# Kernel tuning notes

Measured on AMD Instinct MI355X. Metric: run time of the kernel, lower is better.

## Reference

```python
import jax, jax.numpy as jnp
import numpy as np

B, C, H, W = 8, 512, 32, 32
HEADS, GROUPS, EPS = 8, 32, 1e-5


def setup_inputs() -> dict:
    key = jax.random.key(0)
    ks = jax.random.split(key, 8)
    s = 1.0 / np.sqrt(C)
    return {
        "hidden_states": jax.random.normal(ks[0], (B, C, H, W), jnp.float32),
        "gn_w": jnp.ones((C,), jnp.float32),
        "gn_b": jnp.zeros((C,), jnp.float32),
        "Wq": jax.random.normal(ks[1], (C, C), jnp.float32) * s,
        "Wk": jax.random.normal(ks[2], (C, C), jnp.float32) * s,
        "Wv": jax.random.normal(ks[3], (C, C), jnp.float32) * s,
        "Wo": jax.random.normal(ks[4], (C, C), jnp.float32) * s,
        "bo": jnp.zeros((C,), jnp.float32),
    }


def reference(hidden_states, gn_w, gn_b, Wq, Wk, Wv, Wo, bo):
    b, c, h, w = hidden_states.shape
    S = h * w
    d = c // HEADS
    # [B,C,H,W] -> [B,S,C]
    x = hidden_states.reshape(b, c, S).transpose(0, 2, 1)

    # GroupNorm over channels (applied on [B,C,S] layout): normalize per (group, spatial)
    xt = x.transpose(0, 2, 1).reshape(b, GROUPS, c // GROUPS, S)
    mu = jnp.mean(xt, axis=(2, 3), keepdims=True)
    var = jnp.var(xt, axis=(2, 3), keepdims=True)
    normed = ((xt - mu) * jax.lax.rsqrt(var + EPS)).reshape(b, c, S)
    normed = (normed * gn_w[None, :, None] + gn_b[None, :, None]).transpose(0, 2, 1)  # [B,S,C]

    # Projections: query from normed states, key/value from raw encoder(=hidden) states
    q = (normed @ Wq.T).reshape(b, S, HEADS, d)
    k = (x @ Wk.T).reshape(b, S, HEADS, d)
    v = (x @ Wv.T).reshape(b, S, HEADS, d)

    scale = d ** -0.5
    scores = jnp.einsum("bshd,bthd->bhst", q, k) * scale  # [B,H,S,S]
    probs = jax.nn.softmax(scores.astype(jnp.float32), axis=-1)  # fp32 softmax (also stored)
    ctx = jnp.einsum("bhst,bthd->bshd", probs.astype(v.dtype), v).reshape(b, S, c)

    out = ctx @ Wo.T + bo  # to_out[0]; to_out[1] is dropout (identity at eval)
    return out.transpose(0, 2, 1).reshape(b, c, h, w)
```

## Files before the change

### kernel.cpp

```cpp
#include <hip/hip_runtime.h>
#include <hip/hip_bf16.h>

typedef short bf16x8 __attribute__((ext_vector_type(8)));
typedef short s16x4  __attribute__((ext_vector_type(4)));
typedef float f32x4  __attribute__((ext_vector_type(4)));

#define NB 8
#define NC 512
#define NS 1024
#define NH 8
#define DH 64
#define GN_GROUPS 32
#define GN_EPS 1e-5f

#if __has_builtin(__builtin_amdgcn_exp2f)
#define EXP2(x) __builtin_amdgcn_exp2f(x)
#else
#define EXP2(x) __expf((x) * 0.69314718056f)
#endif

static __device__ __forceinline__ short f2bf(float f) {
  union { __hip_bfloat16 h; short s; } u;
  u.h = __float2bfloat16(f);
  return u.s;
}

static __device__ __forceinline__ int pack2bf_fast(float a, float b) {
  unsigned ua = __float_as_uint(a) + 0x8000u;
  unsigned ub = __float_as_uint(b) + 0x8000u;
  return (int)__builtin_amdgcn_perm(ub, ua, 0x07060302u);
}

static __device__ __forceinline__ void async_lds16(const void* g, void* l) {
  __builtin_amdgcn_global_load_lds((__attribute__((address_space(1))) void*)(g),
                                   (__attribute__((address_space(3))) void*)(l),
                                   16, 0, 0);
}

#define MFMA16(a, b, c) __builtin_amdgcn_mfma_f32_16x16x32_bf16((a), (b), (c), 0, 0, 0)

__global__ __launch_bounds__(256) void prep(const float* __restrict__ x,
                                            float* __restrict__ stats,
                                            const float4* __restrict__ Wq,
                                            const float4* __restrict__ Wk,
                                            const float4* __restrict__ Wv,
                                            const float4* __restrict__ Wo,
                                            s16x4* __restrict__ oq, s16x4* __restrict__ ok,
                                            s16x4* __restrict__ ov, s16x4* __restrict__ oo,
                                            float qscale) {
  if (blockIdx.x < 256) {
    int bg = blockIdx.x;
    const float4* p = (const float4*)(x + (size_t)bg * 16384);
    float s = 0.f, s2 = 0.f;
    for (int i = threadIdx.x; i < 4096; i += 256) {
      float4 v = p[i];
      s  += v.x + v.y + v.z + v.w;
      s2 += v.x * v.x + v.y * v.y + v.z * v.z + v.w * v.w;
    }
    for (int off = 32; off > 0; off >>= 1) {
      s  += __shfl_down(s, off, 64);
      s2 += __shfl_down(s2, off, 64);
    }
    __shared__ float red[8];
    int w = threadIdx.x >> 6;
    if ((threadIdx.x & 63) == 0) { red[w * 2] = s; red[w * 2 + 1] = s2; }
    __syncthreads();
    if (threadIdx.x == 0) {
      float S = 0.f, S2 = 0.f;
      for (int i = 0; i < 4; i++) { S += red[i * 2]; S2 += red[i * 2 + 1]; }
      float mu  = S / 16384.f;
      float var = S2 / 16384.f - mu * mu;
      stats[bg * 2]     = mu;
      stats[bg * 2 + 1] = rsqrtf(var + GN_EPS);
    }
  } else {
    int idx = blockIdx.x - 256;
    int sel = idx >> 8;
    int i = (idx & 255) * 256 + threadIdx.x;
    const float4* src = (sel == 0) ? Wq : (sel == 1) ? Wk : (sel == 2) ? Wv : Wo;
    s16x4* dst        = (sel == 0) ? oq : (sel == 1) ? ok : (sel == 2) ? ov : oo;
    float scale = (sel == 0) ? qscale : 1.0f;
    float4 f = src[i];
    s16x4 o;
    o[0] = f2bf(f.x * scale); o[1] = f2bf(f.y * scale);
    o[2] = f2bf(f.z * scale); o[3] = f2bf(f.w * scale);
    dst[i] = o;
  }
}

__global__ __launch_bounds__(256) void tnorm(const float* __restrict__ x,
                                             const float* __restrict__ stats,
                                             const float* __restrict__ gw,
                                             const float* __restrict__ gb,
                                             short* __restrict__ xT,
                                             short* __restrict__ nT) {
  __shared__ float tile[64 * 65];
  int b = blockIdx.z, c0 = blockIdx.y * 64, s0 = blockIdx.x * 64;
  int t = threadIdx.x;
  const float* xp = x + ((size_t)b * NC + c0) * NS + s0;
#pragma unroll
  for (int p = 0; p < 4; p++) {
    int idx = p * 256 + t;
    int cl = idx >> 4;
    int s4 = (idx & 15) * 4;
    float4 v = *(const float4*)(xp + (size_t)cl * NS + s4);
    tile[cl * 65 + s4 + 0] = v.x;
    tile[cl * 65 + s4 + 1] = v.y;
    tile[cl * 65 + s4 + 2] = v.z;
    tile[cl * 65 + s4 + 3] = v.w;
  }
  __syncthreads();
#pragma unroll
  for (int p = 0; p < 4; p++) {
    int idx = p * 256 + t;
    int sl = idx >> 4;
    int c4 = (idx & 15) * 4;
    size_t ob = ((size_t)b * NS + s0 + sl) * NC + c0 + c4;
    s16x4 xo, no;
#pragma unroll
    for (int j = 0; j < 4; j++) {
      int c = c0 + c4 + j;
      float val = tile[(c4 + j) * 65 + sl];
      int g = c >> 4;
      float mu = stats[(b * GN_GROUPS + g) * 2];
      float rs = stats[(b * GN_GROUPS + g) * 2 + 1];
      float nv = (val - mu) * rs * gw[c] + gb[c];
      xo[j] = f2bf(val);
      no[j] = f2bf(nv);
    }
    *(s16x4*)(xT + ob) = xo;
    *(s16x4*)(nT + ob) = no;
  }
}

__global__ __launch_bounds__(256) void gemm_qkv(const short* __restrict__ nT,
                                                const short* __restrict__ xT,
                                                const short* __restrict__ wq,
                                                const short* __restrict__ wk,
                                                const short* __restrict__ wv,
                                                short* __restrict__ q,
                                                short* __restrict__ k,
                                                short* __restrict__ vt) {
  __shared__ __attribute__((aligned(16))) short smem[8704];
  short* sA = smem;
  short* sB = smem + 4096;
  int proj = blockIdx.y >> 2;
  int n0 = (blockIdx.y & 3) * 128;
  int m0 = blockIdx.x * 128;
  const short* A  = (proj == 0) ? nT : xT;
  const short* Bm = (proj == 0) ? wq : ((proj == 1) ? wk : wv);
  short* Out      = (proj == 0) ? q  : ((proj == 1) ? k  : vt);

  int tid = threadIdx.x, lane = tid & 63, w = tid >> 6;
  int quad = lane >> 4, l16 = lane & 15;
  int m_off = (w >> 1) * 64, n_off = (w & 1) * 64;
  int sr4 = lane >> 2;
  int csw = ((lane & 3) ^ ((sr4 >> 1) & 3)) * 8;
  int rsw = (quad ^ ((l16 >> 1) & 3)) * 8;

  const short* gA = A  + ((size_t)(m0 + w * 32 + sr4)) * 512 + csw;
  const short* gB = Bm + ((size_t)(n0 + w * 32 + sr4)) * 512 + csw;
  short* lA = &sA[w * 1024];
  short* lB = &sB[w * 1024];

  f32x4 acc[4][4] = {};

  for (int kk = 0; kk < 512; kk += 32) {
    __syncthreads();
    async_lds16(gA + kk,            lA);
    async_lds16(gA + kk + 16 * 512, lA + 512);
    async_lds16(gB + kk,            lB);
    async_lds16(gB + kk + 16 * 512, lB + 512);
    __syncthreads();
    bf16x8 aF[4], bF[4];
#pragma unroll
    for (int ms = 0; ms < 4; ms++)
      aF[ms] = *(const bf16x8*)&sA[(m_off + ms * 16 + l16) * 32 + rsw];
#pragma unroll
    for (int ns = 0; ns < 4; ns++)
      bF[ns] = *(const bf16x8*)&sB[(n_off + ns * 16 + l16) * 32 + rsw];
#pragma unroll
    for (int ms = 0; ms < 4; ms++)
#pragma unroll
      for (int ns = 0; ns < 4; ns++)
        acc[ms][ns] = MFMA16(aF[ms], bF[ns], acc[ms][ns]);
  }
  if (proj < 2) {
    short* sT = smem;
    int hown = m_off >> 6;
#pragma unroll
    for (int hm = 0; hm < 2; hm++) {
      __syncthreads();
      if (hown == hm) {
#pragma unroll
        for (int ms = 0; ms < 4; ms++)
#pragma unroll
          for (int ns = 0; ns < 4; ns++)
#pragma unroll
            for (int r = 0; r < 4; r++)
              sT[(ms * 16 + quad * 4 + r) * 136 + n_off + ns * 16 + l16] = f2bf(acc[ms][ns][r]);
      }
      __syncthreads();
#pragma unroll
      for (int p2 = 0; p2 < 4; p2++) {
        int idx = p2 * 256 + tid;
        int row = idx >> 4, ch = (idx & 15) * 8;
        *(bf16x8*)&Out[(size_t)(m0 + hm * 64 + row) * 512 + n0 + ch] =
            *(const bf16x8*)&sT[row * 136 + ch];
      }
    }
  } else {
#pragma unroll
    for (int ms = 0; ms < 4; ms++)
#pragma unroll
      for (int ns = 0; ns < 4; ns++) {
        int rowb = m0 + m_off + ms * 16 + quad * 4;
        int col  = n0 + n_off + ns * 16 + l16;
        int bb = rowb >> 10, s = rowb & 1023;
        s16x4 pk4;
#pragma unroll
        for (int r = 0; r < 4; r++) pk4[r] = f2bf(acc[ms][ns][r]);
        *(s16x4*)&Out[((size_t)(bb * NC + col)) * NS + s] = pk4;
      }
  }
}

__global__ __launch_bounds__(512, 4) void attn(const short* __restrict__ q,
                                               const short* __restrict__ k,
                                               const short* __restrict__ vT,
                                               short* __restrict__ ctx) {
  __shared__ __attribute__((aligned(16))) short smem[32768];
#define SKp(wg, p, hf) (&smem[((wg) * 4 + (p) * 2 + (hf)) * 2048])
#define SVp(wg, p, c)  (&smem[16384 + ((wg) * 4 + (p) * 2 + (c)) * 2048])
  int b = blockIdx.x >> 3, h = blockIdx.x & 7;
  int q0 = blockIdx.y * 128;
  int tid = threadIdx.x, lane = tid & 63, w = tid >> 6;
  int wg = w >> 2, wl = w & 3;
  int quad = lane >> 4, l16 = lane & 15;

  const short* kb = k  + (size_t)b * (NS * NC) + h * DH;
  const short* vb = vT + (size_t)(b * NH + h) * (DH * NS);

  bf16x8 qf[2][2];
#pragma unroll
  for (int g = 0; g < 2; g++) {
    const short* qp = q + ((size_t)(b * NS + q0 + g * 64 + wl * 16 + l16)) * NC + h * DH + quad * 8;
    qf[g][0] = *(const bf16x8*)qp;
    qf[g][1] = *(const bf16x8*)(qp + 32);
  }

  int sr4  = lane >> 2;
  int srow = wl * 16 + sr4;
  int csw  = ((lane & 3) ^ ((sr4 >> 1) & 3)) * 8;
  int rsw  = (quad ^ ((l16 >> 1) & 3)) * 8;

#define STAGE(p, kt) do {                                              \
    int kv0_ = (wg * 8 + (kt)) * 64;                                   \
    const short* kg_ = kb + (size_t)(kv0_ + srow) * NC + csw;          \
    async_lds16(kg_,      SKp(wg, p, 0) + wl * 512);                   \
    async_lds16(kg_ + 32, SKp(wg, p, 1) + wl * 512);                   \
    const short* vg_ = vb + (size_t)srow * NS + kv0_ + csw;            \
    async_lds16(vg_,      SVp(wg, p, 0) + wl * 512);                   \
    async_lds16(vg_ + 32, SVp(wg, p, 1) + wl * 512);                   \
  } while (0)

  STAGE(0, 0);

  f32x4 o[2][4] = {};
  float lsum[2] = {0.f, 0.f};
  int src0 = (quad & 1) * 32 + l16;
  int src1 = src0 + 16;
  int selB = quad >> 1;

  for (int kt = 0; kt < 8; kt++) {
    int p = kt & 1;
    __syncthreads();
    if (kt < 7) STAGE(1 - p, kt + 1);

    f32x4 sc[2][4];
#pragma unroll
    for (int mt = 0; mt < 4; mt++) {
      bf16x8 ak0 = *(const bf16x8*)(SKp(wg, p, 0) + (mt * 16 + l16) * 32 + rsw);
      bf16x8 ak1 = *(const bf16x8*)(SKp(wg, p, 1) + (mt * 16 + l16) * 32 + rsw);
#pragma unroll
      for (int g = 0; g < 2; g++) {
        f32x4 z = {0.f, 0.f, 0.f, 0.f};
        z = MFMA16(ak0, qf[g][0], z);
        z = MFMA16(ak1, qf[g][1], z);
        sc[g][mt] = z;
      }
    }
    int pk[2][4][2];
#pragma unroll
    for (int g = 0; g < 2; g++)
#pragma unroll
      for (int mt = 0; mt < 4; mt++)
#pragma unroll
        for (int hh = 0; hh < 2; hh++) {
          float e0 = EXP2(sc[g][mt][2 * hh]);
          float e1 = EXP2(sc[g][mt][2 * hh + 1]);
          lsum[g] += e0 + e1;
          pk[g][mt][hh] = pack2bf_fast(e0, e1);
        }
    bf16x8 pf[2][2];
#pragma unroll
    for (int g = 0; g < 2; g++)
#pragma unroll
      for (int c = 0; c < 2; c++) {
        union { int d[4]; bf16x8 v; } u;
#pragma unroll
        for (int dd = 0; dd < 4; dd++) {
          int s = (dd >> 1) ? src1 : src0;
          int A = __shfl(pk[g][2 * c][dd & 1], s, 64);
          int B = __shfl(pk[g][2 * c + 1][dd & 1], s, 64);
          u.d[dd] = selB ? B : A;
        }
        pf[g][c] = u.v;
      }
#pragma unroll
    for (int dt = 0; dt < 4; dt++) {
      bf16x8 av0 = *(const bf16x8*)(SVp(wg, p, 0) + (dt * 16 + l16) * 32 + rsw);
      bf16x8 av1 = *(const bf16x8*)(SVp(wg, p, 1) + (dt * 16 + l16) * 32 + rsw);
#pragma unroll
      for (int g = 0; g < 2; g++) {
        o[g][dt] = MFMA16(av0, pf[g][0], o[g][dt]);
        o[g][dt] = MFMA16(av1, pf[g][1], o[g][dt]);
      }
    }
  }
#pragma unroll
  for (int g = 0; g < 2; g++) {
    lsum[g] += __shfl_xor(lsum[g], 16, 64);
    lsum[g] += __shfl_xor(lsum[g], 32, 64);
  }
  float* dump  = (float*)smem;
  float* lsums = (float*)&smem[16384];
  __syncthreads();
  if (wg == 1) {
#pragma unroll
    for (int g = 0; g < 2; g++) {
#pragma unroll
      for (int dt = 0; dt < 4; dt++)
        *(f32x4*)&dump[((((g * 4 + wl) * 4) + dt) * 64 + lane) * 4] = o[g][dt];
      if (quad == 0) lsums[(g * 4 + wl) * 16 + l16] = lsum[g];
    }
  }
  __syncthreads();
  float inv[2];
  if (wg == 0) {
#pragma unroll
    for (int g = 0; g < 2; g++) {
      inv[g] = 1.f / (lsum[g] + lsums[(g * 4 + wl) * 16 + l16]);
#pragma unroll
      for (int dt = 0; dt < 4; dt++) {
        f32x4 add = *(const f32x4*)&dump[((((g * 4 + wl) * 4) + dt) * 64 + lane) * 4];
        o[g][dt] += add;
      }
    }
  }
  __syncthreads();
  short* sT = &smem[0];
  if (wg == 0) {
#pragma unroll
    for (int g = 0; g < 2; g++)
#pragma unroll
      for (int dt = 0; dt < 4; dt++)
#pragma unroll
        for (int r = 0; r < 4; r++)
          sT[(g * 64 + wl * 16 + l16) * 72 + dt * 16 + quad * 4 + r] = f2bf(o[g][dt][r] * inv[g]);
  }
  __syncthreads();
  for (int it = tid; it < 1024; it += 512) {
    int row = it >> 3, ch = (it & 7) * 8;
    *(bf16x8*)&ctx[((size_t)(b * NS + q0 + row)) * NC + h * DH + ch] =
        *(const bf16x8*)&sT[row * 72 + ch];
  }
#undef STAGE
#undef SKp
#undef SVp
}

__global__ __launch_bounds__(256) void gemm_out(const short* __restrict__ ctx,
                                                const short* __restrict__ wo,
                                                const float* __restrict__ bo,
                                                float* __restrict__ out) {
  __shared__ __attribute__((aligned(16))) short sA[64 * 32];
  __shared__ __attribute__((aligned(16))) short sB[128 * 32];
  int n0 = blockIdx.y * 128;
  int m0 = blockIdx.x * 64;
  int tid = threadIdx.x, lane = tid & 63, w = tid >> 6;
  int quad = lane >> 4, l16 = lane & 15;
  int sr4 = lane >> 2;
  int csw = ((lane & 3) ^ ((sr4 >> 1) & 3)) * 8;
  int rsw = (quad ^ ((l16 >> 1) & 3)) * 8;

  const short* gA = ctx + ((size_t)(m0 + w * 16 + sr4)) * 512 + csw;
  const short* gB = wo  + ((size_t)(n0 + w * 32 + sr4)) * 512 + csw;
  short* lA = &sA[w * 512];
  short* lB = &sB[w * 1024];

  f32x4 acc[4][2] = {};

  for (int kk = 0; kk < 512; kk += 32) {
    __syncthreads();
    async_lds16(gA + kk,            lA);
    async_lds16(gB + kk,            lB);
    async_lds16(gB + kk + 16 * 512, lB + 512);
    __syncthreads();
    bf16x8 aF[4], bF[2];
#pragma unroll
    for (int ms = 0; ms < 4; ms++)
      aF[ms] = *(const bf16x8*)&sA[(ms * 16 + l16) * 32 + rsw];
#pragma unroll
    for (int ns = 0; ns < 2; ns++)
      bF[ns] = *(const bf16x8*)&sB[(w * 32 + ns * 16 + l16) * 32 + rsw];
#pragma unroll
    for (int ms = 0; ms < 4; ms++)
#pragma unroll
      for (int ns = 0; ns < 2; ns++)
        acc[ms][ns] = MFMA16(aF[ms], bF[ns], acc[ms][ns]);
  }
#pragma unroll
  for (int ms = 0; ms < 4; ms++)
#pragma unroll
    for (int ns = 0; ns < 2; ns++) {
      int rowb = m0 + ms * 16 + quad * 4;
      int col  = n0 + w * 32 + ns * 16 + l16;
      int bb = rowb >> 10, s = rowb & 1023;
      float bias = bo[col];
      f32x4 vv = acc[ms][ns];
      vv[0] += bias; vv[1] += bias; vv[2] += bias; vv[3] += bias;
      *(f32x4*)&out[((size_t)(bb * NC + col)) * NS + s] = vv;
    }
}

extern "C" void kernel_launch(void* const* d_in, const int* in_sizes, int n_in,
                              void* d_out, int out_size, void* d_ws, size_t ws_size,
                              hipStream_t stream) {
  const float* x  = (const float*)d_in[0];
  const float* gw = (const float*)d_in[1];
  const float* gb = (const float*)d_in[2];
  const float* Wq = (const float*)d_in[3];
  const float* Wk = (const float*)d_in[4];
  const float* Wv = (const float*)d_in[5];
  const float* Wo = (const float*)d_in[6];
  const float* bo = (const float*)d_in[7];
  float* out = (float*)d_out;

  char* ws = (char*)d_ws;
  const size_t MAT = (size_t)8192 * 512 * 2;
  float* stats = (float*)ws;
  short* xT  = (short*)(ws + 4096);
  short* nT  = (short*)(ws + 4096 + 1 * MAT);
  short* q   = (short*)(ws + 4096 + 2 * MAT);
  short* k   = (short*)(ws + 4096 + 3 * MAT);
  short* vt  = (short*)(ws + 4096 + 4 * MAT);
  short* ctx = (short*)(ws + 4096 + 5 * MAT);
  short* wqb = (short*)(ws + 4096 + 6 * MAT);
  short* wkb = wqb + 262144;
  short* wvb = wkb + 262144;
  short* wob = wvb + 262144;

  const float qscale = 0.125f * 1.44269504088896f;
  prep<<<1280, 256, 0, stream>>>(x, stats,
                                 (const float4*)Wq, (const float4*)Wk,
                                 (const float4*)Wv, (const float4*)Wo,
                                 (s16x4*)wqb, (s16x4*)wkb, (s16x4*)wvb, (s16x4*)wob,
                                 qscale);
  tnorm<<<dim3(16, 8, 8), 256, 0, stream>>>(x, stats, gw, gb, xT, nT);
  gemm_qkv<<<dim3(64, 12), 256, 0, stream>>>(nT, xT, wqb, wkb, wvb, q, k, vt);
  attn<<<dim3(64, 8), 512, 0, stream>>>(q, k, vt, ctx);
  gemm_out<<<dim3(128, 4), 256, 0, stream>>>(ctx, wob, bo, out);
}
```

Baseline: 149.4 us.

## Route attention probabilities through LDS and halve the KV tile size

The attention kernel now processes 32 keys per iteration (16 iterations instead of 8), and the LDS footprint shrinks from 64KB to about 52KB. It replaces the cross-lane shuffle transpose of the exp'd scores with a per-wave LDS scratch write followed by a vector read, guarded by an lgkmcnt wait. The goal is to cut shuffle instruction overhead and register pressure, and perhaps to raise occupancy through the smaller shared memory use. In exchange it adds twice as many block-wide barriers and extra LDS traffic per tile.

```diff
diff --git a/kernel.cpp b/kernel.cpp
--- a/kernel.cpp
+++ b/kernel.cpp
@@ -229,9 +229,9 @@
                                                const short* __restrict__ k,
                                                const short* __restrict__ vT,
                                                short* __restrict__ ctx) {
-  __shared__ __attribute__((aligned(16))) short smem[32768];
-#define SKp(wg, p, hf) (&smem[((wg) * 4 + (p) * 2 + (hf)) * 2048])
-#define SVp(wg, p, c)  (&smem[16384 + ((wg) * 4 + (p) * 2 + (c)) * 2048])
+  __shared__ __attribute__((aligned(16))) short smem[26624];
+#define SKh(wg, p, hf) (&smem[((wg) * 4 + (p) * 2 + (hf)) * 1024])
+#define SVp(wg, p)     (&smem[8192 + ((wg) * 2 + (p)) * 2048])
   int b = blockIdx.x >> 3, h = blockIdx.x & 7;
   int q0 = blockIdx.y * 128;
   int tid = threadIdx.x, lane = tid & 63, w = tid >> 6;
@@ -240,6 +240,7 @@
 
   const short* kb = k  + (size_t)b * (NS * NC) + h * DH;
   const short* vb = vT + (size_t)(b * NH + h) * (DH * NS);
+  short* pw = &smem[16384 + w * 1280];
 
   bf16x8 qf[2][2];
 #pragma unroll
@@ -249,39 +250,35 @@
     qf[g][1] = *(const bf16x8*)(qp + 32);
   }
 
-  int sr4  = lane >> 2;
-  int srow = wl * 16 + sr4;
-  int csw  = ((lane & 3) ^ ((sr4 >> 1) & 3)) * 8;
-  int rsw  = (quad ^ ((l16 >> 1) & 3)) * 8;
-
-#define STAGE(p, kt) do {                                              \
-    int kv0_ = (wg * 8 + (kt)) * 64;                                   \
-    const short* kg_ = kb + (size_t)(kv0_ + srow) * NC + csw;          \
-    async_lds16(kg_,      SKp(wg, p, 0) + wl * 512);                   \
-    async_lds16(kg_ + 32, SKp(wg, p, 1) + wl * 512);                   \
-    const short* vg_ = vb + (size_t)srow * NS + kv0_ + csw;            \
-    async_lds16(vg_,      SVp(wg, p, 0) + wl * 512);                   \
-    async_lds16(vg_ + 32, SVp(wg, p, 1) + wl * 512);                   \
+#define STAGE(p, kt) do {                                                  \
+    int kv0_ = wg * 512 + (kt) * 32;                                       \
+    int kr_ = (wl >> 1) * 16 + (lane >> 2);                                \
+    int kc_ = (wl & 1) * 32 + (((lane & 3) ^ ((kr_ >> 1) & 3)) * 8);       \
+    async_lds16(kb + (size_t)(kv0_ + kr_) * NC + kc_,                      \
+                SKh(wg, p, wl & 1) + (wl >> 1) * 512);                     \
+    int vr_ = wl * 16 + (lane >> 2);                                       \
+    int vc_ = ((lane & 3) ^ ((vr_ >> 1) & 3)) * 8;                         \
+    async_lds16(vb + (size_t)vr_ * NS + kv0_ + vc_,                        \
+                SVp(wg, p) + wl * 512);                                    \
   } while (0)
 
   STAGE(0, 0);
 
   f32x4 o[2][4] = {};
   float lsum[2] = {0.f, 0.f};
-  int src0 = (quad & 1) * 32 + l16;
-  int src1 = src0 + 16;
-  int selB = quad >> 1;
-
-  for (int kt = 0; kt < 8; kt++) {
+
+  for (int kt = 0; kt < 16; kt++) {
     int p = kt & 1;
     __syncthreads();
-    if (kt < 7) STAGE(1 - p, kt + 1);
-
-    f32x4 sc[2][4];
-#pragma unroll
-    for (int mt = 0; mt < 4; mt++) {
-      bf16x8 ak0 = *(const bf16x8*)(SKp(wg, p, 0) + (mt * 16 + l16) * 32 + rsw);
-      bf16x8 ak1 = *(const bf16x8*)(SKp(wg, p, 1) + (mt * 16 + l16) * 32 + rsw);
+    if (kt < 15) STAGE(1 - p, kt + 1);
+
+    f32x4 sc[2][2];
+#pragma unroll
+    for (int mt = 0; mt < 2; mt++) {
+      int row = mt * 16 + l16;
+      int fro = row * 32 + ((quad ^ ((row >> 1) & 3)) * 8);
+      bf16x8 ak0 = *(const bf16x8*)(SKh(wg, p, 0) + fro);
+      bf16x8 ak1 = *(const bf16x8*)(SKh(wg, p, 1) + fro);
 #pragma unroll
       for (int g = 0; g < 2; g++) {
         f32x4 z = {0.f, 0.f, 0.f, 0.f};
@@ -290,42 +287,34 @@
         sc[g][mt] = z;
       }
     }
-    int pk[2][4][2];
+#pragma unroll
+    for (int g = 0; g < 2; g++) {
+      int qi = (g * 16 + l16) * 40;
+#pragma unroll
+      for (int mt = 0; mt < 2; mt++) {
+        float e0 = EXP2(sc[g][mt][0]);
+        float e1 = EXP2(sc[g][mt][1]);
+        float e2 = EXP2(sc[g][mt][2]);
+        float e3 = EXP2(sc[g][mt][3]);
+        lsum[g] += (e0 + e1) + (e2 + e3);
+        int2 pr;
+        pr.x = pack2bf_fast(e0, e1);
+        pr.y = pack2bf_fast(e2, e3);
+        *(int2*)&pw[qi + mt * 16 + quad * 4] = pr;
+      }
+    }
+    __builtin_amdgcn_s_waitcnt(0xc07f);
+    bf16x8 pf[2];
 #pragma unroll
     for (int g = 0; g < 2; g++)
-#pragma unroll
-      for (int mt = 0; mt < 4; mt++)
-#pragma unroll
-        for (int hh = 0; hh < 2; hh++) {
-          float e0 = EXP2(sc[g][mt][2 * hh]);
-          float e1 = EXP2(sc[g][mt][2 * hh + 1]);
-          lsum[g] += e0 + e1;
-          pk[g][mt][hh] = pack2bf_fast(e0, e1);
-        }
-    bf16x8 pf[2][2];
-#pragma unroll
-    for (int g = 0; g < 2; g++)
-#pragma unroll
-      for (int c = 0; c < 2; c++) {
-        union { int d[4]; bf16x8 v; } u;
-#pragma unroll
-        for (int dd = 0; dd < 4; dd++) {
-          int s = (dd >> 1) ? src1 : src0;
-          int A = __shfl(pk[g][2 * c][dd & 1], s, 64);
-          int B = __shfl(pk[g][2 * c + 1][dd & 1], s, 64);
-          u.d[dd] = selB ? B : A;
-        }
-        pf[g][c] = u.v;
-      }
+      pf[g] = *(const bf16x8*)&pw[(g * 16 + l16) * 40 + quad * 8];
 #pragma unroll
     for (int dt = 0; dt < 4; dt++) {
-      bf16x8 av0 = *(const bf16x8*)(SVp(wg, p, 0) + (dt * 16 + l16) * 32 + rsw);
-      bf16x8 av1 = *(const bf16x8*)(SVp(wg, p, 1) + (dt * 16 + l16) * 32 + rsw);
-#pragma unroll
-      for (int g = 0; g < 2; g++) {
-        o[g][dt] = MFMA16(av0, pf[g][0], o[g][dt]);
-        o[g][dt] = MFMA16(av1, pf[g][1], o[g][dt]);
-      }
+      int row = dt * 16 + l16;
+      bf16x8 av = *(const bf16x8*)(SVp(wg, p) + row * 32 + ((quad ^ ((row >> 1) & 3)) * 8));
+#pragma unroll
+      for (int g = 0; g < 2; g++)
+        o[g][dt] = MFMA16(av, pf[g], o[g][dt]);
     }
   }
 #pragma unroll
@@ -376,7 +365,7 @@
         *(const bf16x8*)&sT[row * 72 + ch];
   }
 #undef STAGE
-#undef SKp
+#undef SKh
 #undef SVp
 }
 
```

Result: faster. 145.2 us (-2.8%).
